# Performance work log

Hardware: AMD Instinct MI355X
Metric: run time of the kernel (lower is better)

## Reference

```python
import jax, jax.numpy as jnp
import numpy as np

LATENT_DIM = 8
POLY_DEGREE = 5
DATA_DIM = 64
BATCH = 4096
TOTAL_TERMS = sum(LATENT_DIM ** d for d in range(POLY_DEGREE + 1))  # 37449


def _poly_features(z):
    # z: [B, L] -> [B, sum_d L^d] concatenated Kronecker powers, degree 0..D.
    B = z.shape[0]
    feats = [jnp.ones((B, 1), dtype=z.dtype)]  # degree 0
    cur = z  # degree 1: [B, L]
    feats.append(cur)
    for _ in range(2, POLY_DEGREE + 1):
        # kron(cur, z) per sample: outer product then flatten (row-major matches torch.kron)
        cur = (cur[:, :, None] * z[:, None, :]).reshape(B, -1)
        feats.append(cur)
    return jnp.concatenate(feats, axis=1)  # [B, TOTAL_TERMS]


def setup_inputs() -> dict:
    key = jax.random.key(0)
    k1, k2, k3 = jax.random.split(key, 3)
    z = jax.random.normal(k1, (BATCH, LATENT_DIM), dtype=jnp.float32)
    W = jax.random.normal(k2, (DATA_DIM, TOTAL_TERMS), dtype=jnp.float32) / np.sqrt(TOTAL_TERMS)
    b = jax.random.normal(k3, (DATA_DIM,), dtype=jnp.float32)
    return {"z": z, "W": W, "b": b}


def reference(z, W, b):
    feats = _poly_features(z)                 # [B, TOTAL_TERMS]
    return feats @ W.T + b                    # [B, DATA_DIM]
```

## Files before the change

kernel.cpp:

```cpp
#include <hip/hip_runtime.h>


#define TOTAL_TERMS 37449
#define NSTEP 1172
#define MBLK 32
#define KY 21
#define OUT_ELEMS 262144

typedef _Float16 half8 __attribute__((ext_vector_type(8)));
typedef float f32x4 __attribute__((ext_vector_type(4)));

__global__ __launch_bounds__(256) void convert_w(const float* __restrict__ W,
                                                 const float* __restrict__ bias,
                                                 _Float16* __restrict__ Wt) {
    __shared__ _Float16 lds[64][72];
    int tid  = threadIdx.x;
    int lane = tid & 63;
    int nq   = tid >> 6;
    int kb   = blockIdx.x * 64;
    int kp   = kb + lane;

    int o, mode;
    if (kp < 8)           { o = 1 + kp;            mode = 0; }
    else if (kp == 8)     { o = 0;                 mode = 2; }
    else if (kp < 32)     { o = 0;                 mode = 1; }
    else if (kp < 96)     { o = 9    + (kp - 32);  mode = 0; }
    else if (kp < 608)    { o = 73   + (kp - 96);  mode = 0; }
    else if (kp < 4704)   { o = 585  + (kp - 608); mode = 0; }
    else if (kp < 37472)  { o = 4681 + (kp - 4704);mode = 0; }
    else                  { o = 0;                 mode = 1; }

#pragma unroll
    for (int r = 0; r < 16; ++r) {
        int n = r * 4 + nq;
        const float* wrow = W + (size_t)n * TOTAL_TERMS;
        float v;
        if (mode == 1)      v = 0.f;
        else if (mode == 2) v = wrow[0] + bias[n];
        else                v = wrow[o];
        lds[n][lane] = (_Float16)v;
    }
    __syncthreads();

    int quad = lane >> 4, l16 = lane & 15;
    int n = nq * 16 + l16;
#pragma unroll
    for (int sl = 0; sl < 2; ++sl) {
        int kk = sl * 32 + quad * 8;
        half8 hv;
#pragma unroll
        for (int j = 0; j < 8; ++j) hv[j] = lds[n][kk + j];
        int s = (kb >> 5) + sl;
        *(half8*)(Wt + ((size_t)(s * 4 + nq) * 64 + lane) * 8) = hv;
    }
}

__global__ __launch_bounds__(256, 2) void poly_gemm(const float* __restrict__ z,
                                                    const _Float16* __restrict__ Wt,
                                                    float* __restrict__ part,
                                                    float* __restrict__ out,
                                                    int use_atomic) {
    __shared__ __align__(16) _Float16 zm[128][8];
    __shared__ _Float16 zT[8][144];

    int tid  = threadIdx.x;
    int lane = tid & 63;
    int w    = tid >> 6;
    int g    = w >> 1;
    int h    = w & 1;
    int mb   = blockIdx.x;
    int ky   = blockIdx.y;

    const int sb = (ky < 16) ? (147 + 64 * ky)
                 : (ky < 20) ? (19 + 32 * (ky - 16)) : 0;

    const char* gb = (const char*)Wt + (size_t)(sb * 4 + 2 * h) * 1024
                   + (size_t)lane * 16;

    half8 Bk[2][16];
    if (ky < 20) {
#pragma unroll
        for (int ii = 0; ii < 8; ++ii)
#pragma unroll
            for (int k = 0; k < 2; ++k)
                Bk[0][ii * 2 + k] = *(const half8*)(gb + ii * 4096 + k * 1024);
    }

    if (tid < 128) {
        const float* zp = z + ((size_t)(mb * 128 + tid)) * 8;
        float4 a = *(const float4*)zp;
        float4 b4 = *(const float4*)(zp + 4);
        half8 hz;
        hz[0] = (_Float16)a.x;  hz[1] = (_Float16)a.y;
        hz[2] = (_Float16)a.z;  hz[3] = (_Float16)a.w;
        hz[4] = (_Float16)b4.x; hz[5] = (_Float16)b4.y;
        hz[6] = (_Float16)b4.z; hz[7] = (_Float16)b4.w;
        *(half8*)&zm[tid][0] = hz;
#pragma unroll
        for (int j = 0; j < 8; ++j) zT[j][tid] = hz[j];
    }
    __syncthreads();

    int quad = lane >> 4;
    int l16  = lane & 15;
    int mrow[4];
    half8 zv[4];
    _Float16 zq[4], zq4[4];
#pragma unroll
    for (int t = 0; t < 4; ++t) {
        mrow[t] = g * 64 + t * 16 + l16;
        zv[t]   = *(const half8*)&zm[mrow[t]][0];
        zq[t]   = zT[quad][mrow[t]];
        zq4[t]  = zT[quad + 4][mrow[t]];
    }

    f32x4 acc[4][2];
#pragma unroll
    for (int t = 0; t < 4; ++t)
#pragma unroll
        for (int k = 0; k < 2; ++k) acc[t][k] = (f32x4){0.f, 0.f, 0.f, 0.f};

    if (ky < 20) {
        const bool d5     = (ky < 16);
        const int  r2base = d5 ? 4 * ky : 2 * (ky - 16);
        const int  nsc    = d5 ? 4 : 2;

        _Float16 a1[4];
        if (d5) {
            int r1 = (ky >> 1) & 7;
#pragma unroll
            for (int t = 0; t < 4; ++t) a1[t] = zT[r1][mrow[t]];
        }

        for (int sc = 0; sc < nsc; ++sc) {
            int rtop = (r2base + sc) & 7;
            _Float16 gz[4];
#pragma unroll
            for (int t = 0; t < 4; ++t) {
                _Float16 v = zT[rtop][mrow[t]];
                gz[t] = d5 ? (_Float16)(a1[t] * v) : v;
            }
#pragma unroll
            for (int gp = 0; gp < 2; ++gp) {
                const char* gn = gb + 32768;
#pragma unroll
                for (int ii = 0; ii < 8; ++ii)
#pragma unroll
                    for (int k = 0; k < 2; ++k)
                        Bk[gp ^ 1][ii * 2 + k] =
                            *(const half8*)(gn + ii * 4096 + k * 1024);
#pragma unroll
                for (int ii = 0; ii < 8; ++ii) {
                    const int r3 = gp * 4 + (ii >> 1);
                    half8 av[4];
#pragma unroll
                    for (int t = 0; t < 4; ++t) {
                        _Float16 f = gz[t] * zv[t][r3] *
                                     ((ii & 1) ? zq4[t] : zq[t]);
#pragma unroll
                        for (int e = 0; e < 8; ++e) av[t][e] = zv[t][e] * f;
                    }
#pragma unroll
                    for (int t = 0; t < 4; ++t)
#pragma unroll
                        for (int k = 0; k < 2; ++k)
                            acc[t][k] = __builtin_amdgcn_mfma_f32_16x16x32_f16(
                                av[t], Bk[gp][ii * 2 + k], acc[t][k], 0, 0, 0);
                }
                gb += 32768;
            }
        }
    } else {
        const _Float16* base = Wt + (size_t)h * 1024 + (size_t)lane * 8;
        auto loadB = [&](int s, half8* B) {
            const _Float16* p = base + (size_t)s * 2048;
            B[0] = *(const half8*)p;
            B[1] = *(const half8*)(p + 512);
        };
        auto genA = [&](int s, half8* av) {
            if (s == 0) {
#pragma unroll
                for (int t = 0; t < 4; ++t) {
                    if (quad == 0)      av[t] = zv[t];
                    else if (quad == 1) { av[t] = (half8){}; av[t][0] = (_Float16)1.f; }
                    else                av[t] = (half8){};
                }
                return;
            }
            _Float16 f[4];
            if (s >= 3) {
                int u = s - 3;
                int r1 = (u >> 1) & 7;
                int r2 = ((u & 1) << 2) + quad;
#pragma unroll
                for (int t = 0; t < 4; ++t)
                    f[t] = zT[r1][mrow[t]] * zT[r2][mrow[t]];
            } else {
                int r1 = (s - 1) * 4 + quad;
#pragma unroll
                for (int t = 0; t < 4; ++t)
                    f[t] = zT[r1][mrow[t]];
            }
#pragma unroll
            for (int t = 0; t < 4; ++t)
#pragma unroll
                for (int e = 0; e < 8; ++e) av[t][e] = zv[t][e] * f[t];
        };
        auto mfma8 = [&](const half8* av, const half8* B) {
#pragma unroll
            for (int t = 0; t < 4; ++t)
#pragma unroll
                for (int k = 0; k < 2; ++k)
                    acc[t][k] = __builtin_amdgcn_mfma_f32_16x16x32_f16(
                        av[t], B[k], acc[t][k], 0, 0, 0);
        };

        half8 B0[2], B1[2];
        loadB(0, B0);
        loadB(1, B1);
        int s = 0;
        for (; s + 1 < 19; s += 2) {
            half8 av[4];
            genA(s, av);
            mfma8(av, B0);
            if (s + 2 < 19) loadB(s + 2, B0);
            genA(s + 1, av);
            mfma8(av, B1);
            if (s + 3 < 19) loadB(s + 3, B1);
        }
        {
            half8 av[4];
            genA(18, av);
            mfma8(av, B0);
        }
    }

    float* dstbase = use_atomic ? out : (part + (size_t)ky * OUT_ELEMS);
#pragma unroll
    for (int t = 0; t < 4; ++t) {
        int mbase = mb * 128 + g * 64 + t * 16 + quad * 4;
#pragma unroll
        for (int k = 0; k < 2; ++k) {
            int col = h * 32 + k * 16 + l16;
#pragma unroll
            for (int r = 0; r < 4; ++r) {
                size_t idx = (size_t)(mbase + r) * 64 + col;
                if (use_atomic) unsafeAtomicAdd(out + idx, acc[t][k][r]);
                else __builtin_nontemporal_store(acc[t][k][r], dstbase + idx);
            }
        }
    }
}

__global__ __launch_bounds__(256) void reduce_part(const float* __restrict__ part,
                                                   float* __restrict__ out) {
    int gid = blockIdx.x * 256 + threadIdx.x;
    const f32x4* p4 = (const f32x4*)part;
    f32x4 s = (f32x4){0.f, 0.f, 0.f, 0.f};
#pragma unroll
    for (int j = 0; j < KY; ++j)
        s += __builtin_nontemporal_load(p4 + (size_t)j * (OUT_ELEMS / 4) + gid);
    __builtin_nontemporal_store(s, ((f32x4*)out) + gid);
}

extern "C" void kernel_launch(void* const* d_in, const int* in_sizes, int n_in,
                              void* d_out, int out_size, void* d_ws, size_t ws_size,
                              hipStream_t stream) {
    (void)in_sizes; (void)n_in;
    const float* z = (const float*)d_in[0];
    const float* W = (const float*)d_in[1];
    const float* b = (const float*)d_in[2];
    float* out = (float*)d_out;

    const size_t part_bytes = (size_t)KY * OUT_ELEMS * sizeof(float);
    const size_t wt_bytes   = (size_t)(NSTEP + 16) * 2048 * sizeof(_Float16);
    const bool two_phase = ws_size >= part_bytes + wt_bytes;

    float* part;
    _Float16* Wt;
    if (two_phase) {
        part = (float*)d_ws;
        Wt   = (_Float16*)((char*)d_ws + part_bytes);
    } else {
        part = out;
        Wt   = (_Float16*)d_ws;
    }

    if (!two_phase)
        hipMemsetAsync(d_out, 0, (size_t)out_size * sizeof(float), stream);
    hipLaunchKernelGGL(convert_w, dim3(NSTEP / 2), dim3(256), 0, stream, W, b, Wt);
    hipLaunchKernelGGL(poly_gemm, dim3(MBLK, KY), dim3(256), 0, stream,
                       z, Wt, part, out, two_phase ? 0 : 1);
    if (two_phase)
        hipLaunchKernelGGL(reduce_part, dim3(OUT_ELEMS / 4 / 256), dim3(256), 0,
                           stream, part, out);
}
```

Before: 96.87 us.

## Fold degree-4 and low-degree K-slices into the 16 degree-5 split-K blocks

Reduces the split-K grid dimension from 21 to 16 by removing the separate blocks that handled degree-4 terms and low-degree terms. Each remaining block now processes its degree-5 chunk, then an extra degree-4 step and one or two low-degree steps. The aim is uniform work per block, no divergent branches, and fewer partial outputs to reduce. The cost is somewhat longer per-block work and a less overlapped tail of loads.

```diff
diff --git a/kernel.cpp b/kernel.cpp
--- a/kernel.cpp
+++ b/kernel.cpp
@@ -4,7 +4,7 @@
 #define TOTAL_TERMS 37449
 #define NSTEP 1172
 #define MBLK 32
-#define KY 21
+#define KY 16
 #define OUT_ELEMS 262144
 
 typedef _Float16 half8 __attribute__((ext_vector_type(8)));
@@ -71,20 +71,17 @@
     int mb   = blockIdx.x;
     int ky   = blockIdx.y;
 
-    const int sb = (ky < 16) ? (147 + 64 * ky)
-                 : (ky < 20) ? (19 + 32 * (ky - 16)) : 0;
-
-    const char* gb = (const char*)Wt + (size_t)(sb * 4 + 2 * h) * 1024
-                   + (size_t)lane * 16;
+    const char* gb  = (const char*)Wt + (size_t)((147 + 64 * ky) * 4 + 2 * h) * 1024
+                    + (size_t)lane * 16;
+    const char* gb4 = (const char*)Wt + (size_t)((19 + 8 * ky) * 4 + 2 * h) * 1024
+                    + (size_t)lane * 16;
 
     half8 Bk[2][16];
-    if (ky < 20) {
-#pragma unroll
-        for (int ii = 0; ii < 8; ++ii)
-#pragma unroll
-            for (int k = 0; k < 2; ++k)
-                Bk[0][ii * 2 + k] = *(const half8*)(gb + ii * 4096 + k * 1024);
-    }
+#pragma unroll
+    for (int ii = 0; ii < 8; ++ii)
+#pragma unroll
+        for (int k = 0; k < 2; ++k)
+            Bk[0][ii * 2 + k] = *(const half8*)(gb + ii * 4096 + k * 1024);
 
     if (tid < 128) {
         const float* zp = z + ((size_t)(mb * 128 + tid)) * 8;
@@ -120,118 +117,132 @@
 #pragma unroll
         for (int k = 0; k < 2; ++k) acc[t][k] = (f32x4){0.f, 0.f, 0.f, 0.f};
 
-    if (ky < 20) {
-        const bool d5     = (ky < 16);
-        const int  r2base = d5 ? 4 * ky : 2 * (ky - 16);
-        const int  nsc    = d5 ? 4 : 2;
-
-        _Float16 a1[4];
-        if (d5) {
-            int r1 = (ky >> 1) & 7;
-#pragma unroll
-            for (int t = 0; t < 4; ++t) a1[t] = zT[r1][mrow[t]];
-        }
-
-        for (int sc = 0; sc < nsc; ++sc) {
-            int rtop = (r2base + sc) & 7;
-            _Float16 gz[4];
-#pragma unroll
-            for (int t = 0; t < 4; ++t) {
-                _Float16 v = zT[rtop][mrow[t]];
-                gz[t] = d5 ? (_Float16)(a1[t] * v) : v;
-            }
-#pragma unroll
-            for (int gp = 0; gp < 2; ++gp) {
-                const char* gn = gb + 32768;
-#pragma unroll
-                for (int ii = 0; ii < 8; ++ii)
+    _Float16 a1[4];
+#pragma unroll
+    for (int t = 0; t < 4; ++t) a1[t] = zT[ky >> 1][mrow[t]];
+
+    for (int sc = 0; sc < 4; ++sc) {
+        int rtop = (4 * ky + sc) & 7;
+        _Float16 gz[4];
+#pragma unroll
+        for (int t = 0; t < 4; ++t) gz[t] = a1[t] * zT[rtop][mrow[t]];
+#pragma unroll
+        for (int gp = 0; gp < 2; ++gp) {
+            const char* gn = (sc == 3 && gp == 1) ? gb4 : (gb + 32768);
+#pragma unroll
+            for (int ii = 0; ii < 8; ++ii)
+#pragma unroll
+                for (int k = 0; k < 2; ++k)
+                    Bk[gp ^ 1][ii * 2 + k] =
+                        *(const half8*)(gn + ii * 4096 + k * 1024);
+#pragma unroll
+            for (int ii = 0; ii < 8; ++ii) {
+                const int r3 = gp * 4 + (ii >> 1);
+                half8 av[4];
+#pragma unroll
+                for (int t = 0; t < 4; ++t) {
+                    _Float16 f = gz[t] * zv[t][r3] *
+                                 ((ii & 1) ? zq4[t] : zq[t]);
+#pragma unroll
+                    for (int e = 0; e < 8; ++e) av[t][e] = zv[t][e] * f;
+                }
+#pragma unroll
+                for (int t = 0; t < 4; ++t)
 #pragma unroll
                     for (int k = 0; k < 2; ++k)
-                        Bk[gp ^ 1][ii * 2 + k] =
-                            *(const half8*)(gn + ii * 4096 + k * 1024);
-#pragma unroll
-                for (int ii = 0; ii < 8; ++ii) {
-                    const int r3 = gp * 4 + (ii >> 1);
-                    half8 av[4];
-#pragma unroll
-                    for (int t = 0; t < 4; ++t) {
-                        _Float16 f = gz[t] * zv[t][r3] *
-                                     ((ii & 1) ? zq4[t] : zq[t]);
-#pragma unroll
-                        for (int e = 0; e < 8; ++e) av[t][e] = zv[t][e] * f;
-                    }
-#pragma unroll
-                    for (int t = 0; t < 4; ++t)
-#pragma unroll
-                        for (int k = 0; k < 2; ++k)
-                            acc[t][k] = __builtin_amdgcn_mfma_f32_16x16x32_f16(
-                                av[t], Bk[gp][ii * 2 + k], acc[t][k], 0, 0, 0);
-                }
-                gb += 32768;
-            }
-        }
-    } else {
-        const _Float16* base = Wt + (size_t)h * 1024 + (size_t)lane * 8;
-        auto loadB = [&](int s, half8* B) {
-            const _Float16* p = base + (size_t)s * 2048;
-            B[0] = *(const half8*)p;
-            B[1] = *(const half8*)(p + 512);
-        };
-        auto genA = [&](int s, half8* av) {
-            if (s == 0) {
-#pragma unroll
-                for (int t = 0; t < 4; ++t) {
-                    if (quad == 0)      av[t] = zv[t];
-                    else if (quad == 1) { av[t] = (half8){}; av[t][0] = (_Float16)1.f; }
-                    else                av[t] = (half8){};
-                }
-                return;
-            }
-            _Float16 f[4];
-            if (s >= 3) {
-                int u = s - 3;
-                int r1 = (u >> 1) & 7;
-                int r2 = ((u & 1) << 2) + quad;
-#pragma unroll
-                for (int t = 0; t < 4; ++t)
-                    f[t] = zT[r1][mrow[t]] * zT[r2][mrow[t]];
-            } else {
-                int r1 = (s - 1) * 4 + quad;
-#pragma unroll
-                for (int t = 0; t < 4; ++t)
-                    f[t] = zT[r1][mrow[t]];
-            }
-#pragma unroll
-            for (int t = 0; t < 4; ++t)
-#pragma unroll
-                for (int e = 0; e < 8; ++e) av[t][e] = zv[t][e] * f[t];
-        };
-        auto mfma8 = [&](const half8* av, const half8* B) {
+                        acc[t][k] = __builtin_amdgcn_mfma_f32_16x16x32_f16(
+                            av[t], Bk[gp][ii * 2 + k], acc[t][k], 0, 0, 0);
+            }
+            gb += 32768;
+        }
+    }
+
+    {
+        const char* ge0 = (const char*)Wt + (size_t)(ky * 4 + 2 * h) * 1024
+                        + (size_t)lane * 16;
+        Bk[1][0] = *(const half8*)(ge0);
+        Bk[1][1] = *(const half8*)(ge0 + 1024);
+        if (ky < 3) {
+            const char* ge1 = (const char*)Wt
+                            + (size_t)((16 + ky) * 4 + 2 * h) * 1024
+                            + (size_t)lane * 16;
+            Bk[1][2] = *(const half8*)(ge1);
+            Bk[1][3] = *(const half8*)(ge1 + 1024);
+        }
+        const int r3b = (ky & 1) * 4;
+        _Float16 d2z[4][4];
+#pragma unroll
+        for (int j = 0; j < 4; ++j)
+#pragma unroll
+            for (int t = 0; t < 4; ++t) d2z[t][j] = zT[r3b + j][mrow[t]];
+#pragma unroll
+        for (int ii = 0; ii < 8; ++ii) {
+            half8 av[4];
+#pragma unroll
+            for (int t = 0; t < 4; ++t) {
+                _Float16 f = a1[t] * d2z[t][ii >> 1] *
+                             ((ii & 1) ? zq4[t] : zq[t]);
+#pragma unroll
+                for (int e = 0; e < 8; ++e) av[t][e] = zv[t][e] * f;
+            }
 #pragma unroll
             for (int t = 0; t < 4; ++t)
 #pragma unroll
                 for (int k = 0; k < 2; ++k)
                     acc[t][k] = __builtin_amdgcn_mfma_f32_16x16x32_f16(
-                        av[t], B[k], acc[t][k], 0, 0, 0);
-        };
-
-        half8 B0[2], B1[2];
-        loadB(0, B0);
-        loadB(1, B1);
-        int s = 0;
-        for (; s + 1 < 19; s += 2) {
-            half8 av[4];
-            genA(s, av);
-            mfma8(av, B0);
-            if (s + 2 < 19) loadB(s + 2, B0);
-            genA(s + 1, av);
-            mfma8(av, B1);
-            if (s + 3 < 19) loadB(s + 3, B1);
-        }
-        {
-            half8 av[4];
-            genA(18, av);
-            mfma8(av, B0);
+                        av[t], Bk[0][ii * 2 + k], acc[t][k], 0, 0, 0);
+        }
+    }
+
+    {
+        half8 av[4];
+        if (ky == 0) {
+#pragma unroll
+            for (int t = 0; t < 4; ++t) {
+                if (quad == 0)      av[t] = zv[t];
+                else if (quad == 1) { av[t] = (half8){}; av[t][0] = (_Float16)1.f; }
+                else                av[t] = (half8){};
+            }
+        } else if (ky < 3) {
+            int r1 = (ky - 1) * 4 + quad;
+#pragma unroll
+            for (int t = 0; t < 4; ++t) {
+                _Float16 f = zT[r1][mrow[t]];
+#pragma unroll
+                for (int e = 0; e < 8; ++e) av[t][e] = zv[t][e] * f;
+            }
+        } else {
+            int u = ky - 3;
+            int r1 = u >> 1, r2 = ((u & 1) << 2) + quad;
+#pragma unroll
+            for (int t = 0; t < 4; ++t) {
+                _Float16 f = zT[r1][mrow[t]] * zT[r2][mrow[t]];
+#pragma unroll
+                for (int e = 0; e < 8; ++e) av[t][e] = zv[t][e] * f;
+            }
+        }
+#pragma unroll
+        for (int t = 0; t < 4; ++t)
+#pragma unroll
+            for (int k = 0; k < 2; ++k)
+                acc[t][k] = __builtin_amdgcn_mfma_f32_16x16x32_f16(
+                    av[t], Bk[1][k], acc[t][k], 0, 0, 0);
+
+        if (ky < 3) {
+            int u = 13 + ky;
+            int r1 = u >> 1, r2 = ((u & 1) << 2) + quad;
+#pragma unroll
+            for (int t = 0; t < 4; ++t) {
+                _Float16 f = zT[r1][mrow[t]] * zT[r2][mrow[t]];
+#pragma unroll
+                for (int e = 0; e < 8; ++e) av[t][e] = zv[t][e] * f;
+            }
+#pragma unroll
+            for (int t = 0; t < 4; ++t)
+#pragma unroll
+                for (int k = 0; k < 2; ++k)
+                    acc[t][k] = __builtin_amdgcn_mfma_f32_16x16x32_f16(
+                        av[t], Bk[1][2 + k], acc[t][k], 0, 0, 0);
         }
     }
 
```

Result: faster. 92.94 us (-4.1%).

## Fold W over symmetric monomials to shrink GEMM K from 37k to 1.3k

Applied to the files above, without the earlier changes.

Uses the symmetry of Kronecker powers: every permutation of a monomial gets the same feature value, so W columns are summed into 1287 unique-monomial buckets with a LUT and LDS atomics. The GEMM then runs over K=1312 with features built per row in LDS from a constexpr recurrence table. This removes most of the MFMA work and the split-K partial buffer and its reduction. In exchange the fold kernel reads all of W with shared-memory atomics, and it adds a LUT setup launch that runs on every call.

```diff
diff --git a/kernel.cpp b/kernel.cpp
--- a/kernel.cpp
+++ b/kernel.cpp
@@ -2,296 +2,219 @@
 
 
 #define TOTAL_TERMS 37449
-#define NSTEP 1172
-#define MBLK 32
-#define KY 21
-#define OUT_ELEMS 262144
+#define NBUCKET 1287
+#define KPAD 1312
+#define FSTRIDE 1320
+#define LUT_BYTES 76800
 
 typedef _Float16 half8 __attribute__((ext_vector_type(8)));
 typedef float f32x4 __attribute__((ext_vector_type(4)));
 
-__global__ __launch_bounds__(256) void convert_w(const float* __restrict__ W,
-                                                 const float* __restrict__ bias,
-                                                 _Float16* __restrict__ Wt) {
-    __shared__ _Float16 lds[64][72];
-    int tid  = threadIdx.x;
+__device__ __constant__ int KSTART[6] = {0, 1, 9, 73, 585, 4681};
+__device__ __constant__ int BSTART[6] = {0, 1, 9, 45, 165, 495};
+__device__ __constant__ int NTAB[5][8] = {
+    {1, 1, 1, 1, 1, 1, 1, 1},
+    {8, 7, 6, 5, 4, 3, 2, 1},
+    {36, 28, 21, 15, 10, 6, 3, 1},
+    {120, 84, 56, 35, 20, 10, 4, 1},
+    {330, 210, 126, 70, 35, 15, 5, 1}};
+
+__global__ __launch_bounds__(256) void setup_lut(unsigned short* __restrict__ lut) {
+    int k = blockIdx.x * 256 + threadIdx.x;
+    if (k >= TOTAL_TERMS) return;
+    int d = 0;
+#pragma unroll
+    for (int i = 1; i <= 5; ++i)
+        if (k >= KSTART[i]) d = i;
+    int loc = k - KSTART[d];
+    int dg[5] = {0, 0, 0, 0, 0};
+    for (int i = d - 1; i >= 0; --i) { dg[i] = loc & 7; loc >>= 3; }
+    for (int i = 1; i < d; ++i) {
+        int v = dg[i], j = i;
+        while (j > 0 && dg[j - 1] > v) { dg[j] = dg[j - 1]; --j; }
+        dg[j] = v;
+    }
+    int rank = 0, lo = 0;
+    for (int i = 0; i < d; ++i) {
+        int m = d - 1 - i;
+        for (int c = lo; c < dg[i]; ++c) rank += NTAB[m][c];
+        lo = dg[i];
+    }
+    lut[k] = (unsigned short)(BSTART[d] + rank);
+}
+
+__global__ __launch_bounds__(1024) void fold_w(const float* __restrict__ W,
+                                               const float* __restrict__ bias,
+                                               const unsigned short* __restrict__ lut,
+                                               _Float16* __restrict__ Wt) {
+    __shared__ float bucket[KPAD];
+    int tid = threadIdx.x;
+    int n = blockIdx.x;
+    for (int i = tid; i < KPAD; i += 1024) bucket[i] = 0.f;
+    __syncthreads();
+    const float* Wrow = W + (size_t)n * TOTAL_TERMS;
+    for (int base = 0; base < TOTAL_TERMS; base += 16384) {
+        float v[16];
+        int bi[16];
+#pragma unroll
+        for (int j = 0; j < 16; ++j) {
+            int k = base + tid + j * 1024;
+            bool ok = k < TOTAL_TERMS;
+            v[j] = ok ? Wrow[k] : 0.f;
+            bi[j] = ok ? (int)lut[k] : (KPAD - 1);
+        }
+#pragma unroll
+        for (int j = 0; j < 16; ++j)
+            if (v[j] != 0.f) atomicAdd(&bucket[bi[j]], v[j]);
+    }
+    __syncthreads();
+    if (tid == 0) bucket[0] += bias[n];
+    __syncthreads();
+    if (tid < KPAD / 8) {
+        int t = tid;
+        half8 hv;
+#pragma unroll
+        for (int j = 0; j < 8; ++j) hv[j] = (_Float16)bucket[8 * t + j];
+        int s = t >> 2;
+        int lane = (n & 15) + (t & 3) * 16;
+        int h = n >> 4;
+        *(half8*)(Wt + ((size_t)((s * 4 + h) * 64 + lane)) * 8) = hv;
+    }
+}
+
+struct ATab {
+    unsigned int t[1344];
+    constexpr ATab() : t() {
+        int last[1287] = {};
+        last[0] = 0;
+        for (int c = 0; c < 8; ++c) last[1 + c] = c;
+        int starts[6] = {0, 1, 9, 45, 165, 495};
+        int pcnt[6] = {0, 0, 64, 128, 352, 800};
+        int pos = 0;
+        for (int d = 2; d <= 5; ++d) {
+            int ps = starts[d - 1], pe = starts[d];
+            int dest = starts[d];
+            int cnt = 0;
+            for (int p = ps; p < pe; ++p)
+                for (int c = last[p]; c < 8; ++c) {
+                    last[dest] = c;
+                    t[pos++] = (unsigned)p | ((unsigned)c << 11) |
+                               ((unsigned)dest << 15);
+                    ++dest; ++cnt;
+                }
+            for (; cnt < pcnt[d]; ++cnt)
+                t[pos++] = 0u | (0u << 11) | (1311u << 15);
+        }
+    }
+};
+__device__ const ATab A_TAB{};
+
+__global__ __launch_bounds__(512) void poly_gemm(const float* __restrict__ z,
+                                                 const _Float16* __restrict__ Wt,
+                                                 float* __restrict__ out) {
+    __shared__ _Float16 feats[16][FSTRIDE];
+    __shared__ f32x4 sacc[4][64];
+    int tid = threadIdx.x;
     int lane = tid & 63;
-    int nq   = tid >> 6;
-    int kb   = blockIdx.x * 64;
-    int kp   = kb + lane;
-
-    int o, mode;
-    if (kp < 8)           { o = 1 + kp;            mode = 0; }
-    else if (kp == 8)     { o = 0;                 mode = 2; }
-    else if (kp < 32)     { o = 0;                 mode = 1; }
-    else if (kp < 96)     { o = 9    + (kp - 32);  mode = 0; }
-    else if (kp < 608)    { o = 73   + (kp - 96);  mode = 0; }
-    else if (kp < 4704)   { o = 585  + (kp - 608); mode = 0; }
-    else if (kp < 37472)  { o = 4681 + (kp - 4704);mode = 0; }
-    else                  { o = 0;                 mode = 1; }
-
-#pragma unroll
-    for (int r = 0; r < 16; ++r) {
-        int n = r * 4 + nq;
-        const float* wrow = W + (size_t)n * TOTAL_TERMS;
-        float v;
-        if (mode == 1)      v = 0.f;
-        else if (mode == 2) v = wrow[0] + bias[n];
-        else                v = wrow[o];
-        lds[n][lane] = (_Float16)v;
-    }
-    __syncthreads();
-
-    int quad = lane >> 4, l16 = lane & 15;
-    int n = nq * 16 + l16;
-#pragma unroll
-    for (int sl = 0; sl < 2; ++sl) {
-        int kk = sl * 32 + quad * 8;
-        half8 hv;
-#pragma unroll
-        for (int j = 0; j < 8; ++j) hv[j] = lds[n][kk + j];
-        int s = (kb >> 5) + sl;
-        *(half8*)(Wt + ((size_t)(s * 4 + nq) * 64 + lane) * 8) = hv;
-    }
-}
-
-__global__ __launch_bounds__(256, 2) void poly_gemm(const float* __restrict__ z,
-                                                    const _Float16* __restrict__ Wt,
-                                                    float* __restrict__ part,
-                                                    float* __restrict__ out,
-                                                    int use_atomic) {
-    __shared__ __align__(16) _Float16 zm[128][8];
-    __shared__ _Float16 zT[8][144];
-
-    int tid  = threadIdx.x;
-    int lane = tid & 63;
-    int w    = tid >> 6;
-    int g    = w >> 1;
-    int h    = w & 1;
-    int mb   = blockIdx.x;
-    int ky   = blockIdx.y;
-
-    const int sb = (ky < 16) ? (147 + 64 * ky)
-                 : (ky < 20) ? (19 + 32 * (ky - 16)) : 0;
-
-    const char* gb = (const char*)Wt + (size_t)(sb * 4 + 2 * h) * 1024
-                   + (size_t)lane * 16;
-
-    half8 Bk[2][16];
-    if (ky < 20) {
-#pragma unroll
-        for (int ii = 0; ii < 8; ++ii)
-#pragma unroll
-            for (int k = 0; k < 2; ++k)
-                Bk[0][ii * 2 + k] = *(const half8*)(gb + ii * 4096 + k * 1024);
-    }
+    int w = tid >> 6;
+    int h = w & 3;
+    int kh = w >> 2;
+    int mb = blockIdx.x;
+
+    const char* gb = (const char*)Wt + (size_t)(h * 64 + lane) * 16
+                   + (size_t)kh * 4096;
+    half8 Bk[2][8];
+#pragma unroll
+    for (int i = 0; i < 8; ++i)
+        Bk[0][i] = *(const half8*)(gb + (size_t)i * 8192);
 
     if (tid < 128) {
-        const float* zp = z + ((size_t)(mb * 128 + tid)) * 8;
-        float4 a = *(const float4*)zp;
-        float4 b4 = *(const float4*)(zp + 4);
-        half8 hz;
-        hz[0] = (_Float16)a.x;  hz[1] = (_Float16)a.y;
-        hz[2] = (_Float16)a.z;  hz[3] = (_Float16)a.w;
-        hz[4] = (_Float16)b4.x; hz[5] = (_Float16)b4.y;
-        hz[6] = (_Float16)b4.z; hz[7] = (_Float16)b4.w;
-        *(half8*)&zm[tid][0] = hz;
-#pragma unroll
-        for (int j = 0; j < 8; ++j) zT[j][tid] = hz[j];
-    }
-    __syncthreads();
-
-    int quad = lane >> 4;
-    int l16  = lane & 15;
-    int mrow[4];
-    half8 zv[4];
-    _Float16 zq[4], zq4[4];
-#pragma unroll
-    for (int t = 0; t < 4; ++t) {
-        mrow[t] = g * 64 + t * 16 + l16;
-        zv[t]   = *(const half8*)&zm[mrow[t]][0];
-        zq[t]   = zT[quad][mrow[t]];
-        zq4[t]  = zT[quad + 4][mrow[t]];
-    }
-
-    f32x4 acc[4][2];
-#pragma unroll
-    for (int t = 0; t < 4; ++t)
-#pragma unroll
-        for (int k = 0; k < 2; ++k) acc[t][k] = (f32x4){0.f, 0.f, 0.f, 0.f};
-
-    if (ky < 20) {
-        const bool d5     = (ky < 16);
-        const int  r2base = d5 ? 4 * ky : 2 * (ky - 16);
-        const int  nsc    = d5 ? 4 : 2;
-
-        _Float16 a1[4];
-        if (d5) {
-            int r1 = (ky >> 1) & 7;
-#pragma unroll
-            for (int t = 0; t < 4; ++t) a1[t] = zT[r1][mrow[t]];
+        int row = tid >> 3, c = tid & 7;
+        float v = z[(size_t)(mb * 16 + row) * 8 + c];
+        feats[row][1 + c] = (_Float16)v;
+        if (c == 0) feats[row][0] = (_Float16)1.f;
+    }
+
+    int sub = tid & 31, row = tid >> 5;
+    const int PS[4] = {0, 64, 192, 544};
+    const int PTRIP[4] = {2, 4, 11, 25};
+#pragma unroll
+    for (int dd = 0; dd < 4; ++dd) {
+        __syncthreads();
+        int base = PS[dd] + sub;
+#pragma unroll
+        for (int e = 0; e < PTRIP[dd]; ++e) {
+            unsigned v = A_TAB.t[base + (e << 5)];
+            int p = v & 2047;
+            int c = (v >> 11) & 15;
+            int dst = v >> 15;
+            feats[row][dst] = feats[row][p] * feats[row][1 + c];
         }
-
-        for (int sc = 0; sc < nsc; ++sc) {
-            int rtop = (r2base + sc) & 7;
-            _Float16 gz[4];
-#pragma unroll
-            for (int t = 0; t < 4; ++t) {
-                _Float16 v = zT[rtop][mrow[t]];
-                gz[t] = d5 ? (_Float16)(a1[t] * v) : v;
-            }
-#pragma unroll
-            for (int gp = 0; gp < 2; ++gp) {
-                const char* gn = gb + 32768;
-#pragma unroll
-                for (int ii = 0; ii < 8; ++ii)
-#pragma unroll
-                    for (int k = 0; k < 2; ++k)
-                        Bk[gp ^ 1][ii * 2 + k] =
-                            *(const half8*)(gn + ii * 4096 + k * 1024);
-#pragma unroll
-                for (int ii = 0; ii < 8; ++ii) {
-                    const int r3 = gp * 4 + (ii >> 1);
-                    half8 av[4];
-#pragma unroll
-                    for (int t = 0; t < 4; ++t) {
-                        _Float16 f = gz[t] * zv[t][r3] *
-                                     ((ii & 1) ? zq4[t] : zq[t]);
-#pragma unroll
-                        for (int e = 0; e < 8; ++e) av[t][e] = zv[t][e] * f;
-                    }
-#pragma unroll
-                    for (int t = 0; t < 4; ++t)
-#pragma unroll
-                        for (int k = 0; k < 2; ++k)
-                            acc[t][k] = __builtin_amdgcn_mfma_f32_16x16x32_f16(
-                                av[t], Bk[gp][ii * 2 + k], acc[t][k], 0, 0, 0);
-                }
-                gb += 32768;
-            }
-        }
-    } else {
-        const _Float16* base = Wt + (size_t)h * 1024 + (size_t)lane * 8;
-        auto loadB = [&](int s, half8* B) {
-            const _Float16* p = base + (size_t)s * 2048;
-            B[0] = *(const half8*)p;
-            B[1] = *(const half8*)(p + 512);
-        };
-        auto genA = [&](int s, half8* av) {
-            if (s == 0) {
-#pragma unroll
-                for (int t = 0; t < 4; ++t) {
-                    if (quad == 0)      av[t] = zv[t];
-                    else if (quad == 1) { av[t] = (half8){}; av[t][0] = (_Float16)1.f; }
-                    else                av[t] = (half8){};
-                }
-                return;
-            }
-            _Float16 f[4];
-            if (s >= 3) {
-                int u = s - 3;
-                int r1 = (u >> 1) & 7;
-                int r2 = ((u & 1) << 2) + quad;
-#pragma unroll
-                for (int t = 0; t < 4; ++t)
-                    f[t] = zT[r1][mrow[t]] * zT[r2][mrow[t]];
-            } else {
-                int r1 = (s - 1) * 4 + quad;
-#pragma unroll
-                for (int t = 0; t < 4; ++t)
-                    f[t] = zT[r1][mrow[t]];
-            }
-#pragma unroll
-            for (int t = 0; t < 4; ++t)
-#pragma unroll
-                for (int e = 0; e < 8; ++e) av[t][e] = zv[t][e] * f[t];
-        };
-        auto mfma8 = [&](const half8* av, const half8* B) {
-#pragma unroll
-            for (int t = 0; t < 4; ++t)
-#pragma unroll
-                for (int k = 0; k < 2; ++k)
-                    acc[t][k] = __builtin_amdgcn_mfma_f32_16x16x32_f16(
-                        av[t], B[k], acc[t][k], 0, 0, 0);
-        };
-
-        half8 B0[2], B1[2];
-        loadB(0, B0);
-        loadB(1, B1);
-        int s = 0;
-        for (; s + 1 < 19; s += 2) {
-            half8 av[4];
-            genA(s, av);
-            mfma8(av, B0);
-            if (s + 2 < 19) loadB(s + 2, B0);
-            genA(s + 1, av);
-            mfma8(av, B1);
-            if (s + 3 < 19) loadB(s + 3, B1);
-        }
-        {
-            half8 av[4];
-            genA(18, av);
-            mfma8(av, B0);
-        }
-    }
-
-    float* dstbase = use_atomic ? out : (part + (size_t)ky * OUT_ELEMS);
-#pragma unroll
-    for (int t = 0; t < 4; ++t) {
-        int mbase = mb * 128 + g * 64 + t * 16 + quad * 4;
-#pragma unroll
-        for (int k = 0; k < 2; ++k) {
-            int col = h * 32 + k * 16 + l16;
-#pragma unroll
-            for (int r = 0; r < 4; ++r) {
-                size_t idx = (size_t)(mbase + r) * 64 + col;
-                if (use_atomic) unsafeAtomicAdd(out + idx, acc[t][k][r]);
-                else __builtin_nontemporal_store(acc[t][k][r], dstbase + idx);
-            }
-        }
-    }
-}
-
-__global__ __launch_bounds__(256) void reduce_part(const float* __restrict__ part,
-                                                   float* __restrict__ out) {
-    int gid = blockIdx.x * 256 + threadIdx.x;
-    const f32x4* p4 = (const f32x4*)part;
-    f32x4 s = (f32x4){0.f, 0.f, 0.f, 0.f};
-#pragma unroll
-    for (int j = 0; j < KY; ++j)
-        s += __builtin_nontemporal_load(p4 + (size_t)j * (OUT_ELEMS / 4) + gid);
-    __builtin_nontemporal_store(s, ((f32x4*)out) + gid);
+    }
+    __syncthreads();
+    if (sub < 25) feats[row][1287 + sub] = (_Float16)0.f;
+    __syncthreads();
+
+    f32x4 acc0 = {0.f, 0.f, 0.f, 0.f}, acc1 = {0.f, 0.f, 0.f, 0.f};
+    int q = (lane >> 4) & 3;
+    int arow = lane & 15;
+    const _Float16* ap = &feats[arow][kh * 32 + q * 8];
+
+#define STEP(i, bank, slot)                                                    \
+    {                                                                          \
+        half8 av = *(const half8*)(ap + (i) * 64);                             \
+        if ((i) & 1)                                                           \
+            acc1 = __builtin_amdgcn_mfma_f32_16x16x32_f16(av, Bk[bank][slot],  \
+                                                          acc1, 0, 0, 0);      \
+        else                                                                   \
+            acc0 = __builtin_amdgcn_mfma_f32_16x16x32_f16(av, Bk[bank][slot],  \
+                                                          acc0, 0, 0, 0);      \
+    }
+
+#pragma unroll
+    for (int i = 0; i < 8; ++i)
+        Bk[1][i] = *(const half8*)(gb + (size_t)(8 + i) * 8192);
+#pragma unroll
+    for (int i = 0; i < 8; ++i) STEP(i, 0, i)
+#pragma unroll
+    for (int i = 0; i < 4; ++i)
+        Bk[0][i] = *(const half8*)(gb + (size_t)(16 + i) * 8192);
+    if (kh == 0) Bk[0][4] = *(const half8*)(gb + (size_t)20 * 8192);
+#pragma unroll
+    for (int i = 8; i < 16; ++i) STEP(i, 1, i - 8)
+#pragma unroll
+    for (int i = 16; i < 20; ++i) STEP(i, 0, i - 16)
+    if (kh == 0) STEP(20, 0, 4)
+#undef STEP
+
+    f32x4 accf = acc0 + acc1;
+
+    if (kh == 1) sacc[h][lane] = accf;
+    __syncthreads();
+    if (kh == 0) {
+        accf += sacc[h][lane];
+        int col = h * 16 + (lane & 15);
+        int r0 = mb * 16 + q * 4;
+#pragma unroll
+        for (int r = 0; r < 4; ++r)
+            out[(size_t)(r0 + r) * 64 + col] = accf[r];
+    }
 }
 
 extern "C" void kernel_launch(void* const* d_in, const int* in_sizes, int n_in,
                               void* d_out, int out_size, void* d_ws, size_t ws_size,
                               hipStream_t stream) {
-    (void)in_sizes; (void)n_in;
+    (void)in_sizes; (void)n_in; (void)out_size; (void)ws_size;
     const float* z = (const float*)d_in[0];
     const float* W = (const float*)d_in[1];
     const float* b = (const float*)d_in[2];
     float* out = (float*)d_out;
 
-    const size_t part_bytes = (size_t)KY * OUT_ELEMS * sizeof(float);
-    const size_t wt_bytes   = (size_t)(NSTEP + 16) * 2048 * sizeof(_Float16);
-    const bool two_phase = ws_size >= part_bytes + wt_bytes;
-
-    float* part;
-    _Float16* Wt;
-    if (two_phase) {
-        part = (float*)d_ws;
-        Wt   = (_Float16*)((char*)d_ws + part_bytes);
-    } else {
-        part = out;
-        Wt   = (_Float16*)d_ws;
-    }
-
-    if (!two_phase)
-        hipMemsetAsync(d_out, 0, (size_t)out_size * sizeof(float), stream);
-    hipLaunchKernelGGL(convert_w, dim3(NSTEP / 2), dim3(256), 0, stream, W, b, Wt);
-    hipLaunchKernelGGL(poly_gemm, dim3(MBLK, KY), dim3(256), 0, stream,
-                       z, Wt, part, out, two_phase ? 0 : 1);
-    if (two_phase)
-        hipLaunchKernelGGL(reduce_part, dim3(OUT_ELEMS / 4 / 256), dim3(256), 0,
-                           stream, part, out);
-}
+    unsigned short* lut = (unsigned short*)d_ws;
+    _Float16* Wt = (_Float16*)((char*)d_ws + LUT_BYTES);
+
+    hipLaunchKernelGGL(setup_lut, dim3((TOTAL_TERMS + 255) / 256), dim3(256), 0,
+                       stream, lut);
+    hipLaunchKernelGGL(fold_w, dim3(64), dim3(1024), 0, stream, W, b, lut, Wt);
+    hipLaunchKernelGGL(poly_gemm, dim3(256), dim3(512), 0, stream, z, Wt, out);
+}
```

Result: slower. 123.8 us (+27.8%).
